# Kernel tuning notes

Measured on AMD Instinct MI355X. Metric: run time of the kernel, lower is better.

## Reference

```python
import jax, jax.numpy as jnp
import numpy as np
import math

B, H, N, D = 2, 16, 2048, 64

def setup_inputs() -> dict:
    key = jax.random.key(0)
    kq, kk, kv, kb = jax.random.split(key, 4)
    return {
        "query": jax.random.normal(kq, (B, H, N, D), dtype=jnp.float32),
        "key": jax.random.normal(kk, (B, H, N, D), dtype=jnp.float32),
        "value": jax.random.normal(kv, (B, H, N, D), dtype=jnp.float32),
        "relative_position_bias": jax.random.normal(kb, (H, N, N), dtype=jnp.float32),
    }

def reference(query, key, value, relative_position_bias):
    d = query.shape[-1]
    # scores: [B,H,N,N]
    attn = jnp.einsum("bhnd,bhmd->bhnm", query, key) / jnp.sqrt(jnp.asarray(d, query.dtype))
    attn = attn + relative_position_bias[None]  # broadcast over batch
    attn = jax.nn.softmax(attn, axis=-1)
    # dropout p=0.0 -> identity
    output = jnp.einsum("bhnm,bhmd->bhnd", attn, value)
    return (output, attn)
```

## Files before the change

kernel.cpp:

```cpp
#include <hip/hip_runtime.h>
#include <cstdint>

#define BN 2
#define HN 16
#define NN 2048
#define DD 64
#define KT 64
#define NT (NN / KT)
#define LDP 72
#define LDF 68

typedef __attribute__((ext_vector_type(8))) short short8;
typedef __attribute__((ext_vector_type(2))) uint32_t uint2v;
typedef __attribute__((ext_vector_type(4))) uint32_t uint4v;
typedef __attribute__((ext_vector_type(4))) float float4v;

static __device__ __forceinline__ uint32_t cvt_pk_bf16(float a, float b){
    uint32_t r;
    asm("v_cvt_pk_bf16_f32 %0, %1, %2" : "=v"(r) : "v"(a), "v"(b));
    return r;
}
static __device__ __forceinline__ unsigned short f2bf1(float a){
    return (unsigned short)(cvt_pk_bf16(a, a) & 0xffffu);
}

static __device__ __forceinline__ float4v mfma_bf16(short8 a, short8 b, float4v c){
    return __builtin_amdgcn_mfma_f32_16x16x32_bf16(a, b, c, 0, 0, 0);
}

static __device__ __forceinline__ void barrier_lds(){
    asm volatile("s_waitcnt lgkmcnt(0)" ::: "memory");
    __builtin_amdgcn_s_barrier();
    asm volatile("" ::: "memory");
}

__launch_bounds__(256, 4)
__global__ void attn_fused_kernel(const float* __restrict__ Q,
                                  const float* __restrict__ K,
                                  const float* __restrict__ V,
                                  const float* __restrict__ Bias,
                                  float* __restrict__ Out){
    __shared__ unsigned short Kb[KT][LDP];
    __shared__ unsigned short Vt[DD][LDP];
    __shared__ float Pb[4][16][LDF];

    const int raw  = blockIdx.x;
    const int slot = raw & 7;
    const int idx  = raw >> 3;
    const int b    = idx & 1;
    const int ghr  = slot * 64 + (idx >> 1);
    const int h    = ghr >> 5;
    const int rt   = ghr & 31;

    const int tid = threadIdx.x;
    const int l   = tid & 63;
    const int w   = tid >> 6;
    const int lg  = l >> 4;
    const int ll  = l & 15;
    const int vc  = ll * 4;

    const int srow = tid >> 4;
    const int scol = (tid & 15) << 2;
    const int vsw  = ((tid >> 1) & 7) << 3;

    const int qw = rt * 64 + w * 16;
    const size_t bh = (size_t)(b * HN + h);
    const float* Qg = Q + (bh * NN + qw) * DD;
    const float* Kg = K + bh * NN * DD;
    const float* Vg = V + bh * NN * DD;
    const float* BgV = Bias + (size_t)h * NN * NN + (size_t)(qw + lg) * NN + vc;

    short8 qf[2];
    {
        const float* qrow = Qg + (size_t)ll * DD + lg * 8;
        #pragma unroll
        for(int ks = 0; ks < 2; ++ks){
            float4v f0 = *(const float4v*)(qrow + ks * 32);
            float4v f1 = *(const float4v*)(qrow + ks * 32 + 4);
            uint4v u;
            u[0] = cvt_pk_bf16(f0[0], f0[1]);
            u[1] = cvt_pk_bf16(f0[2], f0[3]);
            u[2] = cvt_pk_bf16(f1[0], f1[1]);
            u[3] = cvt_pk_bf16(f1[2], f1[3]);
            qf[ks] = __builtin_bit_cast(short8, u);
        }
    }

    float lsum[4];
    #pragma unroll
    for(int r = 0; r < 4; ++r) lsum[r] = 0.f;

    float4v kreg[4], bv[4];
    #pragma unroll
    for(int i = 0; i < 4; ++i)
        kreg[i] = *(const float4v*)(Kg + (size_t)(srow + 16*i) * DD + scol);
    #pragma unroll
    for(int it = 0; it < 4; ++it)
        bv[it] = *(const float4v*)(BgV + (size_t)(it * 4) * NN);

    for(int ct = 0; ct < NT; ++ct){
        barrier_lds();
        #pragma unroll
        for(int i = 0; i < 4; ++i){
            uint2v t = { cvt_pk_bf16(kreg[i][0], kreg[i][1]),
                         cvt_pk_bf16(kreg[i][2], kreg[i][3]) };
            *(uint2v*)&Kb[srow + 16*i][scol] = t;
        }
        if(ct + 1 < NT){
            #pragma unroll
            for(int i = 0; i < 4; ++i)
                kreg[i] = *(const float4v*)(Kg + (size_t)((ct+1)*KT + srow + 16*i) * DD + scol);
        }
        barrier_lds();

        #pragma unroll
        for(int it = 0; it < 4; ++it)
            *(float4v*)&Pb[w][it*4 + lg][vc] = bv[it];
        if(ct + 1 < NT){
            #pragma unroll
            for(int it = 0; it < 4; ++it)
                bv[it] = *(const float4v*)(BgV + (size_t)(it * 4) * NN + (ct+1)*KT);
        }

        float4v acc[4];
        #pragma unroll
        for(int sub = 0; sub < 4; ++sub) acc[sub] = (float4v){0.f,0.f,0.f,0.f};
        __builtin_amdgcn_s_setprio(1);
        #pragma unroll
        for(int sub = 0; sub < 4; ++sub){
            short8 b0 = *(const short8*)&Kb[sub*16 + ll][lg*8];
            short8 b1 = *(const short8*)&Kb[sub*16 + ll][32 + lg*8];
            acc[sub] = mfma_bf16(qf[0], b0, acc[sub]);
            acc[sub] = mfma_bf16(qf[1], b1, acc[sub]);
        }
        __builtin_amdgcn_s_setprio(0);

        #pragma unroll
        for(int r = 0; r < 4; ++r){
            float e0 = __expf(acc[0][r] * 0.125f + Pb[w][lg*4+r][      ll]);
            float e1 = __expf(acc[1][r] * 0.125f + Pb[w][lg*4+r][16 +  ll]);
            float e2 = __expf(acc[2][r] * 0.125f + Pb[w][lg*4+r][32 +  ll]);
            float e3 = __expf(acc[3][r] * 0.125f + Pb[w][lg*4+r][48 +  ll]);
            lsum[r] += (e0 + e1) + (e2 + e3);
        }
    }

    float rl[4];
    #pragma unroll
    for(int r = 0; r < 4; ++r){
        #pragma unroll
        for(int d = 1; d < 16; d <<= 1) lsum[r] += __shfl_xor(lsum[r], d);
        rl[r] = 1.0f / lsum[r];
    }

    float4v oacc[4];
    #pragma unroll
    for(int ds = 0; ds < 4; ++ds) oacc[ds] = (float4v){0.f,0.f,0.f,0.f};

    float* attnW = Out + (size_t)BN*HN*NN*DD
                 + (bh * NN + qw + lg) * (size_t)NN + vc;

    float4v vreg[4];
    #pragma unroll
    for(int i = 0; i < 4; ++i){
        kreg[i] = *(const float4v*)(Kg + (size_t)(srow + 16*i) * DD + scol);
        vreg[i] = *(const float4v*)(Vg + (size_t)(srow + 16*i) * DD + scol);
    }
    #pragma unroll
    for(int it = 0; it < 4; ++it)
        bv[it] = *(const float4v*)(BgV + (size_t)(it * 4) * NN);

    for(int ct = 0; ct < NT; ++ct){
        barrier_lds();
        #pragma unroll
        for(int i = 0; i < 4; ++i){
            uint2v t = { cvt_pk_bf16(kreg[i][0], kreg[i][1]),
                         cvt_pk_bf16(kreg[i][2], kreg[i][3]) };
            *(uint2v*)&Kb[srow + 16*i][scol] = t;
            #pragma unroll
            for(int j = 0; j < 4; ++j)
                Vt[scol + j][(srow + 16*i) ^ vsw] = f2bf1(vreg[i][j]);
        }
        if(ct + 1 < NT){
            #pragma unroll
            for(int i = 0; i < 4; ++i){
                kreg[i] = *(const float4v*)(Kg + (size_t)((ct+1)*KT + srow + 16*i) * DD + scol);
                vreg[i] = *(const float4v*)(Vg + (size_t)((ct+1)*KT + srow + 16*i) * DD + scol);
            }
        }
        barrier_lds();

        #pragma unroll
        for(int it = 0; it < 4; ++it)
            *(float4v*)&Pb[w][it*4 + lg][vc] = bv[it];
        if(ct + 1 < NT){
            #pragma unroll
            for(int it = 0; it < 4; ++it)
                bv[it] = *(const float4v*)(BgV + (size_t)(it * 4) * NN + (ct+1)*KT);
        }

        float4v acc[4];
        #pragma unroll
        for(int sub = 0; sub < 4; ++sub) acc[sub] = (float4v){0.f,0.f,0.f,0.f};
        __builtin_amdgcn_s_setprio(1);
        #pragma unroll
        for(int sub = 0; sub < 4; ++sub){
            short8 b0 = *(const short8*)&Kb[sub*16 + ll][lg*8];
            short8 b1 = *(const short8*)&Kb[sub*16 + ll][32 + lg*8];
            acc[sub] = mfma_bf16(qf[0], b0, acc[sub]);
            acc[sub] = mfma_bf16(qf[1], b1, acc[sub]);
        }
        __builtin_amdgcn_s_setprio(0);

        #pragma unroll
        for(int sub = 0; sub < 4; ++sub)
            #pragma unroll
            for(int r = 0; r < 4; ++r){
                float sv = acc[sub][r] * 0.125f + Pb[w][lg*4+r][sub*16+ll];
                Pb[w][lg*4+r][sub*16+ll] = __expf(sv) * rl[r];
            }

        short8 pf0, pf1;
        {
            float4v p0 = *(const float4v*)&Pb[w][ll][lg*8];
            float4v p1 = *(const float4v*)&Pb[w][ll][lg*8 + 4];
            float4v p2 = *(const float4v*)&Pb[w][ll][32 + lg*8];
            float4v p3 = *(const float4v*)&Pb[w][ll][32 + lg*8 + 4];
            uint4v u0, u1;
            u0[0] = cvt_pk_bf16(p0[0], p0[1]);
            u0[1] = cvt_pk_bf16(p0[2], p0[3]);
            u0[2] = cvt_pk_bf16(p1[0], p1[1]);
            u0[3] = cvt_pk_bf16(p1[2], p1[3]);
            u1[0] = cvt_pk_bf16(p2[0], p2[1]);
            u1[1] = cvt_pk_bf16(p2[2], p2[3]);
            u1[2] = cvt_pk_bf16(p3[0], p3[1]);
            u1[3] = cvt_pk_bf16(p3[2], p3[3]);
            pf0 = __builtin_bit_cast(short8, u0);
            pf1 = __builtin_bit_cast(short8, u1);
        }

        #pragma unroll
        for(int it = 0; it < 4; ++it){
            float4v pv = *(const float4v*)&Pb[w][it*4 + lg][vc];
            *(float4v*)(attnW + (size_t)(it*4) * NN + ct*KT) = pv;
        }

        __builtin_amdgcn_s_setprio(1);
        #pragma unroll
        for(int ds = 0; ds < 4; ++ds){
            const int rsw = (2*ds + (ll >> 3)) << 3;
            short8 v0 = *(const short8*)&Vt[ds*16 + ll][(lg*8) ^ rsw];
            short8 v1 = *(const short8*)&Vt[ds*16 + ll][(32 + lg*8) ^ rsw];
            oacc[ds] = mfma_bf16(pf0, v0, oacc[ds]);
            oacc[ds] = mfma_bf16(pf1, v1, oacc[ds]);
        }
        __builtin_amdgcn_s_setprio(0);
    }

    float* outG = Out + (bh * NN + qw) * (size_t)DD;
    #pragma unroll
    for(int ds = 0; ds < 4; ++ds)
        #pragma unroll
        for(int r = 0; r < 4; ++r)
            outG[(size_t)(lg*4 + r) * DD + ds*16 + ll] = oacc[ds][r];
}

extern "C" void kernel_launch(void* const* d_in, const int* in_sizes, int n_in,
                              void* d_out, int out_size, void* d_ws, size_t ws_size,
                              hipStream_t stream) {
    const float* q    = (const float*)d_in[0];
    const float* k    = (const float*)d_in[1];
    const float* v    = (const float*)d_in[2];
    const float* bias = (const float*)d_in[3];
    float* out = (float*)d_out;

    dim3 grid(BN * HN * (NN / 64));
    dim3 block(256);
    hipLaunchKernelGGL(attn_fused_kernel, grid, block, 0, stream, q, k, v, bias, out);
}
```

Measured before the change: 324.3 us.

## Load bias directly into registers and stage probabilities in LDS as bf16

Bias values are now read from global memory straight into registers in MFMA accumulator layout, so they are no longer staged through a float LDS buffer. The probability staging buffer becomes packed bf16, which halves LDS use, and launch bounds are raised to allow 5 blocks per CU. The attention output is reconstructed from the bf16-rounded probabilities, which reduces output precision. The bias loads become uncoalesced scalar loads and are no longer prefetched a tile ahead, which may expose memory latency.

```diff
diff --git a/kernel.cpp b/kernel.cpp
--- a/kernel.cpp
+++ b/kernel.cpp
@@ -8,7 +8,7 @@
 #define KT 64
 #define NT (NN / KT)
 #define LDP 72
-#define LDF 68
+#define LDH 36
 
 typedef __attribute__((ext_vector_type(8))) short short8;
 typedef __attribute__((ext_vector_type(2))) uint32_t uint2v;
@@ -34,7 +34,7 @@
     asm volatile("" ::: "memory");
 }
 
-__launch_bounds__(256, 4)
+__launch_bounds__(256, 5)
 __global__ void attn_fused_kernel(const float* __restrict__ Q,
                                   const float* __restrict__ K,
                                   const float* __restrict__ V,
@@ -42,7 +42,7 @@
                                   float* __restrict__ Out){
     __shared__ unsigned short Kb[KT][LDP];
     __shared__ unsigned short Vt[DD][LDP];
-    __shared__ float Pb[4][16][LDF];
+    __shared__ uint32_t Pbh[4][16][LDH];
 
     const int raw  = blockIdx.x;
     const int slot = raw & 7;
@@ -68,7 +68,7 @@
     const float* Qg = Q + (bh * NN + qw) * DD;
     const float* Kg = K + bh * NN * DD;
     const float* Vg = V + bh * NN * DD;
-    const float* BgV = Bias + (size_t)h * NN * NN + (size_t)(qw + lg) * NN + vc;
+    const float* BgA = Bias + (size_t)h * NN * NN + (size_t)(qw + lg * 4) * NN + ll;
 
     short8 qf[2];
     {
@@ -90,13 +90,10 @@
     #pragma unroll
     for(int r = 0; r < 4; ++r) lsum[r] = 0.f;
 
-    float4v kreg[4], bv[4];
+    float4v kreg[4];
     #pragma unroll
     for(int i = 0; i < 4; ++i)
         kreg[i] = *(const float4v*)(Kg + (size_t)(srow + 16*i) * DD + scol);
-    #pragma unroll
-    for(int it = 0; it < 4; ++it)
-        bv[it] = *(const float4v*)(BgV + (size_t)(it * 4) * NN);
 
     for(int ct = 0; ct < NT; ++ct){
         barrier_lds();
@@ -106,21 +103,18 @@
                          cvt_pk_bf16(kreg[i][2], kreg[i][3]) };
             *(uint2v*)&Kb[srow + 16*i][scol] = t;
         }
+        float bb[16];
+        #pragma unroll
+        for(int sub = 0; sub < 4; ++sub)
+            #pragma unroll
+            for(int r = 0; r < 4; ++r)
+                bb[sub*4+r] = BgA[(size_t)r * NN + ct*KT + sub*16];
         if(ct + 1 < NT){
             #pragma unroll
             for(int i = 0; i < 4; ++i)
                 kreg[i] = *(const float4v*)(Kg + (size_t)((ct+1)*KT + srow + 16*i) * DD + scol);
         }
         barrier_lds();
-
-        #pragma unroll
-        for(int it = 0; it < 4; ++it)
-            *(float4v*)&Pb[w][it*4 + lg][vc] = bv[it];
-        if(ct + 1 < NT){
-            #pragma unroll
-            for(int it = 0; it < 4; ++it)
-                bv[it] = *(const float4v*)(BgV + (size_t)(it * 4) * NN + (ct+1)*KT);
-        }
 
         float4v acc[4];
         #pragma unroll
@@ -137,10 +131,10 @@
 
         #pragma unroll
         for(int r = 0; r < 4; ++r){
-            float e0 = __expf(acc[0][r] * 0.125f + Pb[w][lg*4+r][      ll]);
-            float e1 = __expf(acc[1][r] * 0.125f + Pb[w][lg*4+r][16 +  ll]);
-            float e2 = __expf(acc[2][r] * 0.125f + Pb[w][lg*4+r][32 +  ll]);
-            float e3 = __expf(acc[3][r] * 0.125f + Pb[w][lg*4+r][48 +  ll]);
+            float e0 = __expf(acc[0][r] * 0.125f + bb[r]);
+            float e1 = __expf(acc[1][r] * 0.125f + bb[4+r]);
+            float e2 = __expf(acc[2][r] * 0.125f + bb[8+r]);
+            float e3 = __expf(acc[3][r] * 0.125f + bb[12+r]);
             lsum[r] += (e0 + e1) + (e2 + e3);
         }
     }
@@ -166,9 +160,6 @@
         kreg[i] = *(const float4v*)(Kg + (size_t)(srow + 16*i) * DD + scol);
         vreg[i] = *(const float4v*)(Vg + (size_t)(srow + 16*i) * DD + scol);
     }
-    #pragma unroll
-    for(int it = 0; it < 4; ++it)
-        bv[it] = *(const float4v*)(BgV + (size_t)(it * 4) * NN);
 
     for(int ct = 0; ct < NT; ++ct){
         barrier_lds();
@@ -181,6 +172,12 @@
             for(int j = 0; j < 4; ++j)
                 Vt[scol + j][(srow + 16*i) ^ vsw] = f2bf1(vreg[i][j]);
         }
+        float bb[16];
+        #pragma unroll
+        for(int sub = 0; sub < 4; ++sub)
+            #pragma unroll
+            for(int r = 0; r < 4; ++r)
+                bb[sub*4+r] = BgA[(size_t)r * NN + ct*KT + sub*16];
         if(ct + 1 < NT){
             #pragma unroll
             for(int i = 0; i < 4; ++i){
@@ -189,15 +186,6 @@
             }
         }
         barrier_lds();
-
-        #pragma unroll
-        for(int it = 0; it < 4; ++it)
-            *(float4v*)&Pb[w][it*4 + lg][vc] = bv[it];
-        if(ct + 1 < NT){
-            #pragma unroll
-            for(int it = 0; it < 4; ++it)
-                bv[it] = *(const float4v*)(BgV + (size_t)(it * 4) * NN + (ct+1)*KT);
-        }
 
         float4v acc[4];
         #pragma unroll
@@ -216,32 +204,23 @@
         for(int sub = 0; sub < 4; ++sub)
             #pragma unroll
             for(int r = 0; r < 4; ++r){
-                float sv = acc[sub][r] * 0.125f + Pb[w][lg*4+r][sub*16+ll];
-                Pb[w][lg*4+r][sub*16+ll] = __expf(sv) * rl[r];
+                float p = __expf(acc[sub][r] * 0.125f + bb[sub*4+r]) * rl[r];
+                ((unsigned short*)&Pbh[w][lg*4 + r][0])[sub*16 + ll] = f2bf1(p);
             }
 
-        short8 pf0, pf1;
-        {
-            float4v p0 = *(const float4v*)&Pb[w][ll][lg*8];
-            float4v p1 = *(const float4v*)&Pb[w][ll][lg*8 + 4];
-            float4v p2 = *(const float4v*)&Pb[w][ll][32 + lg*8];
-            float4v p3 = *(const float4v*)&Pb[w][ll][32 + lg*8 + 4];
-            uint4v u0, u1;
-            u0[0] = cvt_pk_bf16(p0[0], p0[1]);
-            u0[1] = cvt_pk_bf16(p0[2], p0[3]);
-            u0[2] = cvt_pk_bf16(p1[0], p1[1]);
-            u0[3] = cvt_pk_bf16(p1[2], p1[3]);
-            u1[0] = cvt_pk_bf16(p2[0], p2[1]);
-            u1[1] = cvt_pk_bf16(p2[2], p2[3]);
-            u1[2] = cvt_pk_bf16(p3[0], p3[1]);
-            u1[3] = cvt_pk_bf16(p3[2], p3[3]);
-            pf0 = __builtin_bit_cast(short8, u0);
-            pf1 = __builtin_bit_cast(short8, u1);
-        }
+        asm volatile("s_waitcnt lgkmcnt(0)" ::: "memory");
+
+        short8 pf0 = __builtin_bit_cast(short8, *(const uint4v*)&Pbh[w][ll][lg*4]);
+        short8 pf1 = __builtin_bit_cast(short8, *(const uint4v*)&Pbh[w][ll][16 + lg*4]);
 
         #pragma unroll
         for(int it = 0; it < 4; ++it){
-            float4v pv = *(const float4v*)&Pb[w][it*4 + lg][vc];
+            uint2v pw = *(const uint2v*)&Pbh[w][lg + 4*it][ll*2];
+            float4v pv;
+            pv[0] = __builtin_bit_cast(float, pw[0] << 16);
+            pv[1] = __builtin_bit_cast(float, pw[0] & 0xffff0000u);
+            pv[2] = __builtin_bit_cast(float, pw[1] << 16);
+            pv[3] = __builtin_bit_cast(float, pw[1] & 0xffff0000u);
             *(float4v*)(attnW + (size_t)(it*4) * NN + ct*KT) = pv;
         }
 
```

After: 566.5 us. 1.75x slower.

## Double-buffer K/V tiles in LDS and widen blocks to 128 query rows

Applied to the files above, without the earlier changes.

Blocks grow from 4 to 8 waves and cover 128 query rows, so each K/V tile staged in LDS is shared by twice as many rows and global K/V traffic per row is halved. K and V tiles are double-buffered, with registers prefetching two tiles ahead, which drops one of the two barriers per iteration. The block-to-(head, batch, row-tile) mapping is reordered so that blocks of the same head stay grouped for bias reuse. In exchange, LDS use per block roughly doubles, and the larger blocks at 4 blocks/CU may raise register pressure or lower occupancy.

```diff
diff --git a/kernel.cpp b/kernel.cpp
--- a/kernel.cpp
+++ b/kernel.cpp
@@ -7,6 +7,7 @@
 #define DD 64
 #define KT 64
 #define NT (NN / KT)
+#define QB 128
 #define LDP 72
 #define LDF 68
 
@@ -23,6 +24,14 @@
 static __device__ __forceinline__ unsigned short f2bf1(float a){
     return (unsigned short)(cvt_pk_bf16(a, a) & 0xffffu);
 }
+static __device__ __forceinline__ short8 pack8(float4v f0, float4v f1){
+    uint4v u;
+    u[0] = cvt_pk_bf16(f0[0], f0[1]);
+    u[1] = cvt_pk_bf16(f0[2], f0[3]);
+    u[2] = cvt_pk_bf16(f1[0], f1[1]);
+    u[3] = cvt_pk_bf16(f1[2], f1[3]);
+    return __builtin_bit_cast(short8, u);
+}
 
 static __device__ __forceinline__ float4v mfma_bf16(short8 a, short8 b, float4v c){
     return __builtin_amdgcn_mfma_f32_16x16x32_bf16(a, b, c, 0, 0, 0);
@@ -34,23 +43,23 @@
     asm volatile("" ::: "memory");
 }
 
-__launch_bounds__(256, 4)
+__launch_bounds__(512, 4)
 __global__ void attn_fused_kernel(const float* __restrict__ Q,
                                   const float* __restrict__ K,
                                   const float* __restrict__ V,
                                   const float* __restrict__ Bias,
                                   float* __restrict__ Out){
-    __shared__ unsigned short Kb[KT][LDP];
-    __shared__ unsigned short Vt[DD][LDP];
-    __shared__ float Pb[4][16][LDF];
+    __shared__ unsigned short Kb[2][KT][LDP];
+    __shared__ unsigned short Vt[2][DD][LDP];
+    __shared__ float Pb[8][16][LDF];
 
     const int raw  = blockIdx.x;
     const int slot = raw & 7;
     const int idx  = raw >> 3;
-    const int b    = idx & 1;
-    const int ghr  = slot * 64 + (idx >> 1);
-    const int h    = ghr >> 5;
-    const int rt   = ghr & 31;
+    const int h    = slot * 2 + (idx >> 5);
+    const int rem  = idx & 31;
+    const int b    = rem & 1;
+    const int rt   = rem >> 1;
 
     const int tid = threadIdx.x;
     const int l   = tid & 63;
@@ -63,7 +72,7 @@
     const int scol = (tid & 15) << 2;
     const int vsw  = ((tid >> 1) & 7) << 3;
 
-    const int qw = rt * 64 + w * 16;
+    const int qw = rt * QB + w * 16;
     const size_t bh = (size_t)(b * HN + h);
     const float* Qg = Q + (bh * NN + qw) * DD;
     const float* Kg = K + bh * NN * DD;
@@ -74,45 +83,48 @@
     {
         const float* qrow = Qg + (size_t)ll * DD + lg * 8;
         #pragma unroll
-        for(int ks = 0; ks < 2; ++ks){
-            float4v f0 = *(const float4v*)(qrow + ks * 32);
-            float4v f1 = *(const float4v*)(qrow + ks * 32 + 4);
-            uint4v u;
-            u[0] = cvt_pk_bf16(f0[0], f0[1]);
-            u[1] = cvt_pk_bf16(f0[2], f0[3]);
-            u[2] = cvt_pk_bf16(f1[0], f1[1]);
-            u[3] = cvt_pk_bf16(f1[2], f1[3]);
-            qf[ks] = __builtin_bit_cast(short8, u);
-        }
+        for(int ks = 0; ks < 2; ++ks)
+            qf[ks] = pack8(*(const float4v*)(qrow + ks * 32),
+                           *(const float4v*)(qrow + ks * 32 + 4));
     }
 
     float lsum[4];
     #pragma unroll
     for(int r = 0; r < 4; ++r) lsum[r] = 0.f;
 
-    float4v kreg[4], bv[4];
-    #pragma unroll
-    for(int i = 0; i < 4; ++i)
-        kreg[i] = *(const float4v*)(Kg + (size_t)(srow + 16*i) * DD + scol);
+    float4v kreg[2], bv[4];
+    #pragma unroll
+    for(int i = 0; i < 2; ++i)
+        kreg[i] = *(const float4v*)(Kg + (size_t)(srow + 32*i) * DD + scol);
+    #pragma unroll
+    for(int i = 0; i < 2; ++i){
+        uint2v t = { cvt_pk_bf16(kreg[i][0], kreg[i][1]),
+                     cvt_pk_bf16(kreg[i][2], kreg[i][3]) };
+        *(uint2v*)&Kb[0][srow + 32*i][scol] = t;
+    }
+    #pragma unroll
+    for(int i = 0; i < 2; ++i)
+        kreg[i] = *(const float4v*)(Kg + (size_t)(KT + srow + 32*i) * DD + scol);
     #pragma unroll
     for(int it = 0; it < 4; ++it)
         bv[it] = *(const float4v*)(BgV + (size_t)(it * 4) * NN);
+    barrier_lds();
 
     for(int ct = 0; ct < NT; ++ct){
-        barrier_lds();
-        #pragma unroll
-        for(int i = 0; i < 4; ++i){
-            uint2v t = { cvt_pk_bf16(kreg[i][0], kreg[i][1]),
-                         cvt_pk_bf16(kreg[i][2], kreg[i][3]) };
-            *(uint2v*)&Kb[srow + 16*i][scol] = t;
-        }
+        const int cur = ct & 1;
         if(ct + 1 < NT){
             #pragma unroll
-            for(int i = 0; i < 4; ++i)
-                kreg[i] = *(const float4v*)(Kg + (size_t)((ct+1)*KT + srow + 16*i) * DD + scol);
-        }
-        barrier_lds();
-
+            for(int i = 0; i < 2; ++i){
+                uint2v t = { cvt_pk_bf16(kreg[i][0], kreg[i][1]),
+                             cvt_pk_bf16(kreg[i][2], kreg[i][3]) };
+                *(uint2v*)&Kb[cur ^ 1][srow + 32*i][scol] = t;
+            }
+        }
+        if(ct + 2 < NT){
+            #pragma unroll
+            for(int i = 0; i < 2; ++i)
+                kreg[i] = *(const float4v*)(Kg + (size_t)((ct+2)*KT + srow + 32*i) * DD + scol);
+        }
         #pragma unroll
         for(int it = 0; it < 4; ++it)
             *(float4v*)&Pb[w][it*4 + lg][vc] = bv[it];
@@ -128,8 +140,8 @@
         __builtin_amdgcn_s_setprio(1);
         #pragma unroll
         for(int sub = 0; sub < 4; ++sub){
-            short8 b0 = *(const short8*)&Kb[sub*16 + ll][lg*8];
-            short8 b1 = *(const short8*)&Kb[sub*16 + ll][32 + lg*8];
+            short8 b0 = *(const short8*)&Kb[cur][sub*16 + ll][lg*8];
+            short8 b1 = *(const short8*)&Kb[cur][sub*16 + ll][32 + lg*8];
             acc[sub] = mfma_bf16(qf[0], b0, acc[sub]);
             acc[sub] = mfma_bf16(qf[1], b1, acc[sub]);
         }
@@ -143,6 +155,7 @@
             float e3 = __expf(acc[3][r] * 0.125f + Pb[w][lg*4+r][48 +  ll]);
             lsum[r] += (e0 + e1) + (e2 + e3);
         }
+        barrier_lds();
     }
 
     float rl[4];
@@ -160,36 +173,51 @@
     float* attnW = Out + (size_t)BN*HN*NN*DD
                  + (bh * NN + qw + lg) * (size_t)NN + vc;
 
-    float4v vreg[4];
-    #pragma unroll
-    for(int i = 0; i < 4; ++i){
-        kreg[i] = *(const float4v*)(Kg + (size_t)(srow + 16*i) * DD + scol);
-        vreg[i] = *(const float4v*)(Vg + (size_t)(srow + 16*i) * DD + scol);
+    float4v vreg[2];
+    #pragma unroll
+    for(int i = 0; i < 2; ++i){
+        kreg[i] = *(const float4v*)(Kg + (size_t)(srow + 32*i) * DD + scol);
+        vreg[i] = *(const float4v*)(Vg + (size_t)(srow + 32*i) * DD + scol);
+    }
+    #pragma unroll
+    for(int i = 0; i < 2; ++i){
+        uint2v t = { cvt_pk_bf16(kreg[i][0], kreg[i][1]),
+                     cvt_pk_bf16(kreg[i][2], kreg[i][3]) };
+        *(uint2v*)&Kb[0][srow + 32*i][scol] = t;
+        #pragma unroll
+        for(int j = 0; j < 4; ++j)
+            Vt[0][scol + j][(srow + 32*i) ^ vsw] = f2bf1(vreg[i][j]);
+    }
+    #pragma unroll
+    for(int i = 0; i < 2; ++i){
+        kreg[i] = *(const float4v*)(Kg + (size_t)(KT + srow + 32*i) * DD + scol);
+        vreg[i] = *(const float4v*)(Vg + (size_t)(KT + srow + 32*i) * DD + scol);
     }
     #pragma unroll
     for(int it = 0; it < 4; ++it)
         bv[it] = *(const float4v*)(BgV + (size_t)(it * 4) * NN);
+    barrier_lds();
 
     for(int ct = 0; ct < NT; ++ct){
-        barrier_lds();
-        #pragma unroll
-        for(int i = 0; i < 4; ++i){
-            uint2v t = { cvt_pk_bf16(kreg[i][0], kreg[i][1]),
-                         cvt_pk_bf16(kreg[i][2], kreg[i][3]) };
-            *(uint2v*)&Kb[srow + 16*i][scol] = t;
-            #pragma unroll
-            for(int j = 0; j < 4; ++j)
-                Vt[scol + j][(srow + 16*i) ^ vsw] = f2bf1(vreg[i][j]);
-        }
+        const int cur = ct & 1;
         if(ct + 1 < NT){
             #pragma unroll
-            for(int i = 0; i < 4; ++i){
-                kreg[i] = *(const float4v*)(Kg + (size_t)((ct+1)*KT + srow + 16*i) * DD + scol);
-                vreg[i] = *(const float4v*)(Vg + (size_t)((ct+1)*KT + srow + 16*i) * DD + scol);
+            for(int i = 0; i < 2; ++i){
+                uint2v t = { cvt_pk_bf16(kreg[i][0], kreg[i][1]),
+                             cvt_pk_bf16(kreg[i][2], kreg[i][3]) };
+                *(uint2v*)&Kb[cur ^ 1][srow + 32*i][scol] = t;
+                #pragma unroll
+                for(int j = 0; j < 4; ++j)
+                    Vt[cur ^ 1][scol + j][(srow + 32*i) ^ vsw] = f2bf1(vreg[i][j]);
             }
         }
-        barrier_lds();
-
+        if(ct + 2 < NT){
+            #pragma unroll
+            for(int i = 0; i < 2; ++i){
+                kreg[i] = *(const float4v*)(Kg + (size_t)((ct+2)*KT + srow + 32*i) * DD + scol);
+                vreg[i] = *(const float4v*)(Vg + (size_t)((ct+2)*KT + srow + 32*i) * DD + scol);
+            }
+        }
         #pragma unroll
         for(int it = 0; it < 4; ++it)
             *(float4v*)&Pb[w][it*4 + lg][vc] = bv[it];
@@ -205,8 +233,8 @@
         __builtin_amdgcn_s_setprio(1);
         #pragma unroll
         for(int sub = 0; sub < 4; ++sub){
-            short8 b0 = *(const short8*)&Kb[sub*16 + ll][lg*8];
-            short8 b1 = *(const short8*)&Kb[sub*16 + ll][32 + lg*8];
+            short8 b0 = *(const short8*)&Kb[cur][sub*16 + ll][lg*8];
+            short8 b1 = *(const short8*)&Kb[cur][sub*16 + ll][32 + lg*8];
             acc[sub] = mfma_bf16(qf[0], b0, acc[sub]);
             acc[sub] = mfma_bf16(qf[1], b1, acc[sub]);
         }
@@ -226,17 +254,8 @@
             float4v p1 = *(const float4v*)&Pb[w][ll][lg*8 + 4];
             float4v p2 = *(const float4v*)&Pb[w][ll][32 + lg*8];
             float4v p3 = *(const float4v*)&Pb[w][ll][32 + lg*8 + 4];
-            uint4v u0, u1;
-            u0[0] = cvt_pk_bf16(p0[0], p0[1]);
-            u0[1] = cvt_pk_bf16(p0[2], p0[3]);
-            u0[2] = cvt_pk_bf16(p1[0], p1[1]);
-            u0[3] = cvt_pk_bf16(p1[2], p1[3]);
-            u1[0] = cvt_pk_bf16(p2[0], p2[1]);
-            u1[1] = cvt_pk_bf16(p2[2], p2[3]);
-            u1[2] = cvt_pk_bf16(p3[0], p3[1]);
-            u1[3] = cvt_pk_bf16(p3[2], p3[3]);
-            pf0 = __builtin_bit_cast(short8, u0);
-            pf1 = __builtin_bit_cast(short8, u1);
+            pf0 = pack8(p0, p1);
+            pf1 = pack8(p2, p3);
         }
 
         #pragma unroll
@@ -249,12 +268,14 @@
         #pragma unroll
         for(int ds = 0; ds < 4; ++ds){
             const int rsw = (2*ds + (ll >> 3)) << 3;
-            short8 v0 = *(const short8*)&Vt[ds*16 + ll][(lg*8) ^ rsw];
-            short8 v1 = *(const short8*)&Vt[ds*16 + ll][(32 + lg*8) ^ rsw];
+            short8 v0 = *(const short8*)&Vt[cur][ds*16 + ll][(lg*8) ^ rsw];
+            short8 v1 = *(const short8*)&Vt[cur][ds*16 + ll][(32 + lg*8) ^ rsw];
             oacc[ds] = mfma_bf16(pf0, v0, oacc[ds]);
             oacc[ds] = mfma_bf16(pf1, v1, oacc[ds]);
         }
         __builtin_amdgcn_s_setprio(0);
+
+        barrier_lds();
     }
 
     float* outG = Out + (bh * NN + qw) * (size_t)DD;
@@ -274,7 +295,7 @@
     const float* bias = (const float*)d_in[3];
     float* out = (float*)d_out;
 
-    dim3 grid(BN * HN * (NN / 64));
-    dim3 block(256);
+    dim3 grid(BN * HN * (NN / QB));
+    dim3 block(512);
     hipLaunchKernelGGL(attn_fused_kernel, grid, block, 0, stream, q, k, v, bias, out);
 }
```

Result: faster. 290.8 us (-10.3%).
